# Performance work log

Measured on AMD Instinct MI355X. Metric: run time of the kernel, lower is better.

Reference implementation:

```python
import jax, jax.numpy as jnp
import numpy as np

D = 2048
B, L = 4, 4096

def log_g(x):
    # where(x>=0, log(relu(x)+0.5), -softplus(-x))
    return jnp.where(x >= 0, jnp.log(jax.nn.relu(x) + 0.5), -jax.nn.softplus(-x))

def setup_inputs() -> dict:
    key = jax.random.key(0)
    kx, kz, kn = jax.random.split(key, 3)
    x = jax.random.normal(kx, (B, L, D), dtype=jnp.float32)
    # kaiming_normal for Linear(D, D): std = sqrt(2 / fan_in)
    std = np.sqrt(2.0 / D).astype(np.float32)
    Wz = jax.random.normal(kz, (D, D), dtype=jnp.float32) * std
    Wn = jax.random.normal(kn, (D, D), dtype=jnp.float32) * std
    bz = jnp.zeros((D,), dtype=jnp.float32)
    bn = jnp.zeros((D,), dtype=jnp.float32)
    return {"x": x, "Wz": Wz, "bz": bz, "Wn": Wn, "bn": bn}

def reference(x, Wz, bz, Wn, bn):
    Bq, Lq, Dq = x.shape
    k = jnp.einsum('bld,ed->ble', x, Wz) + bz          # fc_z(x)
    log_z = -jax.nn.softplus(-k)                        # log sigmoid(k)
    log_coeffs = -jax.nn.softplus(k)                    # log(1 - sigmoid(k))
    log_h0 = jnp.full((Bq, 1, Dq), jnp.log(0.5), dtype=x.dtype)  # log_g(0)
    log_h_ = log_g(jnp.einsum('bld,ed->ble', x, Wn) + bn)        # log_g(fc_n(x))
    log_values = jnp.concatenate([log_h0, log_z + log_h_], axis=1)   # (B, L+1, D)
    a_star = jnp.pad(jnp.cumsum(log_coeffs, axis=1), ((0, 0), (1, 0), (0, 0)))  # (B, L+1, D)
    log_h = a_star + jax.lax.cumlogsumexp(log_values - a_star, axis=1)
    return jnp.exp(log_h)[:, 1:]
```

## Files before the change

### kernel.cpp

```cpp
#include <hip/hip_runtime.h>
#include <hip/hip_bf16.h>


#define D_DIM 2048
#define B_DIM 4
#define L_DIM 4096
#define M_DIM (B_DIM * L_DIM)
#define KDIM  D_DIM
#define NCOL  (2 * D_DIM)
#define CHUNK 64
#define NCHUNK (L_DIM / CHUNK)

typedef __bf16 bf16x8 __attribute__((ext_vector_type(8)));
typedef float  f32x4  __attribute__((ext_vector_type(4)));

__device__ __forceinline__ unsigned short f2bf(float f) {
  unsigned int u = __float_as_uint(f);
  u += 0x7FFFu + ((u >> 16) & 1u);
  return (unsigned short)(u >> 16);
}
__device__ __forceinline__ float bf2f(unsigned short s) {
  return __uint_as_float(((unsigned int)s) << 16);
}

__device__ __forceinline__ void load_lds16(const void* g, void* l) {
  __builtin_amdgcn_global_load_lds(
      (const __attribute__((address_space(1))) void*)g,
      (__attribute__((address_space(3))) void*)l, 16, 0, 0);
}

__global__ __launch_bounds__(256) void cast_inputs(
    const float* __restrict__ x, const float* __restrict__ Wz,
    const float* __restrict__ Wn,
    unsigned short* __restrict__ xb, unsigned short* __restrict__ wb) {
  const size_t MK4 = (size_t)M_DIM * KDIM / 4;
  const size_t DD4 = (size_t)D_DIM * D_DIM / 4;
  size_t i = (size_t)blockIdx.x * 256 + threadIdx.x;
  const float4* src; ushort4* dst; size_t off;
  if (i < MK4)            { src = (const float4*)x;  dst = (ushort4*)xb; off = i; }
  else if (i < MK4 + DD4) { src = (const float4*)Wz; dst = (ushort4*)wb; off = i - MK4; }
  else                    { src = (const float4*)Wn;
                            dst = (ushort4*)(wb + (size_t)D_DIM * D_DIM);
                            off = i - MK4 - DD4; }
  float4 v = src[off];
  ushort4 o;
  o.x = f2bf(v.x); o.y = f2bf(v.y); o.z = f2bf(v.z); o.w = f2bf(v.w);
  dst[off] = o;
}

__global__ __launch_bounds__(256) void gemm_fused(
    const unsigned short* __restrict__ xb, const unsigned short* __restrict__ wb,
    const float* __restrict__ bzv, const float* __restrict__ bnv,
    unsigned short* __restrict__ Ab, unsigned short* __restrict__ Gb) {
  __shared__ unsigned short As[128 * 32];
  __shared__ unsigned short Bs[128 * 32];
  const int t = threadIdx.x;
  const int w = t >> 6, lane = t & 63;
  const int ntile = blockIdx.x;
  const int mtile = blockIdx.y;
  const unsigned short* aSrc = xb + (size_t)mtile * 128 * KDIM;
  const unsigned short* bSrc = wb + (size_t)ntile * 128 * KDIM;

  f32x4 acc[4][4] = {};
  const int waveM = (w >> 1) * 64;
  const int waveN = (w & 1) * 64;
  const int r0 = t >> 2, r1 = (t + 256) >> 2, sseg = t & 3;

  for (int k0 = 0; k0 < KDIM; k0 += 32) {
    load_lds16(aSrc + (size_t)r0 * KDIM + k0 + sseg * 8, As + (size_t)t * 8);
    load_lds16(aSrc + (size_t)r1 * KDIM + k0 + sseg * 8, As + (size_t)(t + 256) * 8);
    load_lds16(bSrc + (size_t)r0 * KDIM + k0 + sseg * 8, Bs + (size_t)t * 8);
    load_lds16(bSrc + (size_t)r1 * KDIM + k0 + sseg * 8, Bs + (size_t)(t + 256) * 8);
    __syncthreads();

    bf16x8 aF[4], bF[4];
#pragma unroll
    for (int m = 0; m < 4; ++m)
      aF[m] = *(const bf16x8*)&As[(waveM + m * 16 + (lane & 15)) * 32 + (lane >> 4) * 8];
#pragma unroll
    for (int n = 0; n < 4; ++n)
      bF[n] = *(const bf16x8*)&Bs[(waveN + n * 16 + (lane & 15)) * 32 + (lane >> 4) * 8];
#pragma unroll
    for (int m = 0; m < 4; ++m)
#pragma unroll
      for (int n = 0; n < 4; ++n)
        acc[m][n] = __builtin_amdgcn_mfma_f32_16x16x32_bf16(aF[m], bF[n], acc[m][n], 0, 0, 0);
    __syncthreads();
  }

  const bool isZ = (ntile < 16);
  const int colBase = ntile * 128 + waveN;
  const int rowBase = mtile * 128 + waveM;
#pragma unroll
  for (int n = 0; n < 4; ++n) {
    const int gc = colBase + n * 16 + (lane & 15);
    const int dcol = isZ ? gc : (gc - D_DIM);
    const float bias = isZ ? bzv[dcol] : bnv[dcol];
#pragma unroll
    for (int m = 0; m < 4; ++m) {
      const int gr = rowBase + m * 16 + ((lane >> 4) << 2);
#pragma unroll
      for (int j = 0; j < 4; ++j) {
        const float val = acc[m][n][j] + bias;
        const size_t off = (size_t)(gr + j) * D_DIM + dcol;
        if (isZ) {
          Ab[off] = f2bf(1.0f / (1.0f + __expf(val)));
        } else {
          Gb[off] = f2bf(val >= 0.0f ? val + 0.5f : 1.0f / (1.0f + __expf(-val)));
        }
      }
    }
  }
}

__global__ __launch_bounds__(256) void scan_pass1(
    const unsigned short* __restrict__ Ab, const unsigned short* __restrict__ Gb,
    float* __restrict__ SA, float* __restrict__ SV) {
  const int tid = blockIdx.x * 256 + threadIdx.x;
  const int d = tid & (D_DIM - 1);
  const int c = (tid >> 11) & (NCHUNK - 1);
  const int b = tid >> 17;
  size_t base = ((size_t)b * L_DIM + (size_t)c * CHUNK) * D_DIM + d;
  float Acc = 1.0f, Vcc = 0.0f;
#pragma unroll 8
  for (int i = 0; i < CHUNK; ++i) {
    float a = bf2f(Ab[base + (size_t)i * D_DIM]);
    float g = bf2f(Gb[base + (size_t)i * D_DIM]);
    Vcc = a * Vcc + (1.0f - a) * g;
    Acc *= a;
  }
  SA[tid] = Acc;
  SV[tid] = Vcc;
}

__global__ __launch_bounds__(256) void scan_pass2(
    const float* __restrict__ SA, const float* __restrict__ SV,
    float* __restrict__ H0) {
  const int tid = blockIdx.x * 256 + threadIdx.x;
  const int d = tid & (D_DIM - 1);
  const int b = tid >> 11;
  float h = 0.5f;
  for (int c = 0; c < NCHUNK; ++c) {
    size_t idx = ((size_t)b * NCHUNK + c) * D_DIM + d;
    H0[idx] = h;
    h = SA[idx] * h + SV[idx];
  }
}

__global__ __launch_bounds__(256) void scan_pass3(
    const unsigned short* __restrict__ Ab, const unsigned short* __restrict__ Gb,
    const float* __restrict__ H0, float* __restrict__ out) {
  const int tid = blockIdx.x * 256 + threadIdx.x;
  const int d = tid & (D_DIM - 1);
  const int c = (tid >> 11) & (NCHUNK - 1);
  const int b = tid >> 17;
  size_t base = ((size_t)b * L_DIM + (size_t)c * CHUNK) * D_DIM + d;
  float h = H0[tid];
#pragma unroll 8
  for (int i = 0; i < CHUNK; ++i) {
    float a = bf2f(Ab[base + (size_t)i * D_DIM]);
    float g = bf2f(Gb[base + (size_t)i * D_DIM]);
    h = a * h + (1.0f - a) * g;
    out[base + (size_t)i * D_DIM] = h;
  }
}

extern "C" void kernel_launch(void* const* d_in, const int* in_sizes, int n_in,
                              void* d_out, int out_size, void* d_ws, size_t ws_size,
                              hipStream_t stream) {
  const float* x  = (const float*)d_in[0];
  const float* Wz = (const float*)d_in[1];
  const float* bz = (const float*)d_in[2];
  const float* Wn = (const float*)d_in[3];
  const float* bn = (const float*)d_in[4];
  float* out = (float*)d_out;

  char* ws = (char*)d_ws;
  unsigned short* xb = (unsigned short*)(ws);
  unsigned short* wb = (unsigned short*)(ws + 67108864);
  unsigned short* Ab = (unsigned short*)(ws + 83886080);
  unsigned short* Gb = (unsigned short*)(ws + 150994944);
  float* SA = (float*)(ws + 218103808);
  float* SV = (float*)(ws + 220200960);
  float* H0 = (float*)(ws + 222298112);

  cast_inputs<<<40960, 256, 0, stream>>>(x, Wz, Wn, xb, wb);
  gemm_fused<<<dim3(32, 128), 256, 0, stream>>>(xb, wb, bz, bn, Ab, Gb);
  scan_pass1<<<2048, 256, 0, stream>>>(Ab, Gb, SA, SV);
  scan_pass2<<<32, 256, 0, stream>>>(SA, SV, H0);
  scan_pass3<<<2048, 256, 0, stream>>>(Ab, Gb, H0, out);
}
```

Measured before the change: 659.2 us.

## Rewrite GEMM as 256x256 double-buffered pipelined tile and vectorize scan passes

The GEMM kernel moves from 128x128 tiles with a single LDS buffer and a k-step of 32 to 256x256 tiles with 8 waves, a k-step of 64 and double-buffered LDS. Global-to-LDS loads are staged one and two iterations ahead, LDS layouts are XOR-swizzled, MFMA phases are split into quadrants with barriers and setprio, and block IDs are swizzled. The intent is to overlap memory latency with MFMA work, raise data reuse and avoid LDS bank conflicts. The scan passes now process two adjacent channels per thread using 32-bit loads and float2 stores, which halves the thread count and widens memory accesses.

```diff
diff --git a/kernel.cpp b/kernel.cpp
--- a/kernel.cpp
+++ b/kernel.cpp
@@ -7,7 +7,7 @@
 #define L_DIM 4096
 #define M_DIM (B_DIM * L_DIM)
 #define KDIM  D_DIM
-#define NCOL  (2 * D_DIM)
+#define NT    (KDIM / 64)
 #define CHUNK 64
 #define NCHUNK (L_DIM / CHUNK)
 
@@ -48,89 +48,172 @@
   dst[off] = o;
 }
 
-__global__ __launch_bounds__(256) void gemm_fused(
+__global__ __launch_bounds__(512, 2) void gemm_fused(
     const unsigned short* __restrict__ xb, const unsigned short* __restrict__ wb,
     const float* __restrict__ bzv, const float* __restrict__ bnv,
     unsigned short* __restrict__ Ab, unsigned short* __restrict__ Gb) {
-  __shared__ unsigned short As[128 * 32];
-  __shared__ unsigned short Bs[128 * 32];
+  __shared__ unsigned short lds[2][4][8192];
   const int t = threadIdx.x;
-  const int w = t >> 6, lane = t & 63;
-  const int ntile = blockIdx.x;
-  const int mtile = blockIdx.y;
-  const unsigned short* aSrc = xb + (size_t)mtile * 128 * KDIM;
-  const unsigned short* bSrc = wb + (size_t)ntile * 128 * KDIM;
-
-  f32x4 acc[4][4] = {};
-  const int waveM = (w >> 1) * 64;
-  const int waveN = (w & 1) * 64;
-  const int r0 = t >> 2, r1 = (t + 256) >> 2, sseg = t & 3;
-
-  for (int k0 = 0; k0 < KDIM; k0 += 32) {
-    load_lds16(aSrc + (size_t)r0 * KDIM + k0 + sseg * 8, As + (size_t)t * 8);
-    load_lds16(aSrc + (size_t)r1 * KDIM + k0 + sseg * 8, As + (size_t)(t + 256) * 8);
-    load_lds16(bSrc + (size_t)r0 * KDIM + k0 + sseg * 8, Bs + (size_t)t * 8);
-    load_lds16(bSrc + (size_t)r1 * KDIM + k0 + sseg * 8, Bs + (size_t)(t + 256) * 8);
-    __syncthreads();
-
-    bf16x8 aF[4], bF[4];
-#pragma unroll
-    for (int m = 0; m < 4; ++m)
-      aF[m] = *(const bf16x8*)&As[(waveM + m * 16 + (lane & 15)) * 32 + (lane >> 4) * 8];
-#pragma unroll
-    for (int n = 0; n < 4; ++n)
-      bF[n] = *(const bf16x8*)&Bs[(waveN + n * 16 + (lane & 15)) * 32 + (lane >> 4) * 8];
-#pragma unroll
-    for (int m = 0; m < 4; ++m)
-#pragma unroll
-      for (int n = 0; n < 4; ++n)
-        acc[m][n] = __builtin_amdgcn_mfma_f32_16x16x32_bf16(aF[m], bF[n], acc[m][n], 0, 0, 0);
-    __syncthreads();
-  }
-
-  const bool isZ = (ntile < 16);
-  const int colBase = ntile * 128 + waveN;
-  const int rowBase = mtile * 128 + waveM;
-#pragma unroll
-  for (int n = 0; n < 4; ++n) {
-    const int gc = colBase + n * 16 + (lane & 15);
-    const int dcol = isZ ? gc : (gc - D_DIM);
-    const float bias = isZ ? bzv[dcol] : bnv[dcol];
+  const int lane = t & 63;
+  const int wid = t >> 6;
+  const int wm = wid >> 2, wn = wid & 3;
+  const int laneRow = lane & 15, lg = lane >> 4;
+
+  const int bid = blockIdx.x;
+  const int swz = (bid & 7) * 128 + (bid >> 3);
+  const int mtile = swz >> 4;
+  const int ntile = swz & 15;
+
+  const unsigned short* aBase = xb + (size_t)mtile * 256 * KDIM;
+  const unsigned short* bBase = wb + (size_t)ntile * 256 * KDIM;
+
+  const int r0 = t >> 3;
+  const int sSwz = (t & 7) ^ (r0 & 7);
+
+#define STAGE(buf, reg, srcB, halfRow, kt) do {                                   \
+    const unsigned short* s_ = (srcB) + (size_t)((halfRow) + r0) * KDIM           \
+                               + (kt) * 64 + sSwz * 8;                            \
+    unsigned short* d_ = &lds[buf][reg][t * 8];                                   \
+    load_lds16(s_, d_);                                                           \
+    load_lds16(s_ + 64 * KDIM, d_ + 4096);                                        \
+  } while (0)
+
+  const int sA0 = ((0 + lg) ^ (laneRow & 7)) * 8;
+  const int sA1 = ((4 + lg) ^ (laneRow & 7)) * 8;
+  const int bRow0 = (wn & 1) * 64;
+
+  f32x4 acc[8][4] = {};
+
+  STAGE(0, 2, bBase, 0, 0);  STAGE(0, 3, bBase, 128, 0);
+  STAGE(0, 0, aBase, 0, 0);  STAGE(0, 1, aBase, 128, 0);
+  STAGE(1, 2, bBase, 0, 1);  STAGE(1, 3, bBase, 128, 1);
+  asm volatile("s_waitcnt vmcnt(4)" ::: "memory");
+  __builtin_amdgcn_sched_barrier(0);
+  __builtin_amdgcn_s_barrier();
+
+#define MFMA_QUAD(qm, qn)                                                         \
+  _Pragma("unroll") for (int m = 0; m < 4; ++m)                                   \
+  _Pragma("unroll") for (int n = 0; n < 2; ++n)                                   \
+  _Pragma("unroll") for (int k = 0; k < 2; ++k)                                   \
+    acc[(qm)*4 + m][(qn)*2 + n] = __builtin_amdgcn_mfma_f32_16x16x32_bf16(        \
+        aF[m*2 + k], bF[((qn)*2 + n)*2 + k], acc[(qm)*4 + m][(qn)*2 + n], 0, 0, 0)
+
+  for (int U = 0; U < NT; ++U) {
+    const int cur = U & 1;
+    const unsigned short* ldsA = lds[cur][wm];
+    const unsigned short* ldsB = lds[cur][2 + (wn >> 1)];
+    bf16x8 aF[8], bF[8];
+
 #pragma unroll
     for (int m = 0; m < 4; ++m) {
-      const int gr = rowBase + m * 16 + ((lane >> 4) << 2);
+      aF[m*2+0] = *(const bf16x8*)&ldsA[(m*16 + laneRow) * 64 + sA0];
+      aF[m*2+1] = *(const bf16x8*)&ldsA[(m*16 + laneRow) * 64 + sA1];
+    }
+#pragma unroll
+    for (int n = 0; n < 2; ++n) {
+      bF[n*2+0] = *(const bf16x8*)&ldsB[(bRow0 + n*16 + laneRow) * 64 + sA0];
+      bF[n*2+1] = *(const bf16x8*)&ldsB[(bRow0 + n*16 + laneRow) * 64 + sA1];
+    }
+    if (U + 1 < NT) STAGE(cur ^ 1, 0, aBase, 0, U + 1);
+    __builtin_amdgcn_s_barrier();
+    __builtin_amdgcn_s_setprio(1);
+    MFMA_QUAD(0, 0);
+    __builtin_amdgcn_s_setprio(0);
+    __builtin_amdgcn_s_barrier();
+
+#pragma unroll
+    for (int n = 0; n < 2; ++n) {
+      bF[4 + n*2+0] = *(const bf16x8*)&ldsB[(bRow0 + 32 + n*16 + laneRow) * 64 + sA0];
+      bF[4 + n*2+1] = *(const bf16x8*)&ldsB[(bRow0 + 32 + n*16 + laneRow) * 64 + sA1];
+    }
+    if (U + 1 < NT) STAGE(cur ^ 1, 1, aBase, 128, U + 1);
+    __builtin_amdgcn_s_barrier();
+    __builtin_amdgcn_s_setprio(1);
+    MFMA_QUAD(0, 1);
+    __builtin_amdgcn_s_setprio(0);
+    __builtin_amdgcn_s_barrier();
+
+#pragma unroll
+    for (int m = 0; m < 4; ++m) {
+      aF[m*2+0] = *(const bf16x8*)&ldsA[(64 + m*16 + laneRow) * 64 + sA0];
+      aF[m*2+1] = *(const bf16x8*)&ldsA[(64 + m*16 + laneRow) * 64 + sA1];
+    }
+    if (U + 2 < NT) STAGE(cur, 2, bBase, 0, U + 2);
+    __builtin_amdgcn_s_barrier();
+    __builtin_amdgcn_s_setprio(1);
+    MFMA_QUAD(1, 0);
+    __builtin_amdgcn_s_setprio(0);
+    __builtin_amdgcn_s_barrier();
+
+    if (U + 2 < NT) {
+      STAGE(cur, 3, bBase, 128, U + 2);
+      asm volatile("s_waitcnt vmcnt(4)" ::: "memory");
+      __builtin_amdgcn_sched_barrier(0);
+    } else if (U + 1 < NT) {
+      asm volatile("s_waitcnt vmcnt(0)" ::: "memory");
+      __builtin_amdgcn_sched_barrier(0);
+    }
+    __builtin_amdgcn_s_barrier();
+    __builtin_amdgcn_s_setprio(1);
+    MFMA_QUAD(1, 1);
+    __builtin_amdgcn_s_setprio(0);
+    __builtin_amdgcn_s_barrier();
+  }
+
+  const int gcB = ntile * 256 + wn * 64;
+  const int grB = mtile * 256 + wm * 128;
+  const bool isZ = (ntile < 8);
+  unsigned short* outP = isZ ? Ab : Gb;
+  float bias[4];
+#pragma unroll
+  for (int ni = 0; ni < 4; ++ni) {
+    const int gc = gcB + ni * 16 + laneRow;
+    bias[ni] = isZ ? bzv[gc] : bnv[gc - D_DIM];
+  }
+#pragma unroll
+  for (int mi = 0; mi < 8; ++mi) {
+#pragma unroll
+    for (int ni = 0; ni < 4; ++ni) {
+      const int gc = gcB + ni * 16 + laneRow;
+      const int dcol = isZ ? gc : gc - D_DIM;
 #pragma unroll
       for (int j = 0; j < 4; ++j) {
-        const float val = acc[m][n][j] + bias;
-        const size_t off = (size_t)(gr + j) * D_DIM + dcol;
-        if (isZ) {
-          Ab[off] = f2bf(1.0f / (1.0f + __expf(val)));
-        } else {
-          Gb[off] = f2bf(val >= 0.0f ? val + 0.5f : 1.0f / (1.0f + __expf(-val)));
-        }
+        const float val = acc[mi][ni][j] + bias[ni];
+        const int gr = grB + mi * 16 + (lg << 2) + j;
+        const size_t off = (size_t)gr * D_DIM + dcol;
+        if (isZ) outP[off] = f2bf(1.0f / (1.0f + __expf(val)));
+        else     outP[off] = f2bf(val >= 0.0f ? val + 0.5f
+                                              : 1.0f / (1.0f + __expf(-val)));
       }
     }
   }
+#undef STAGE
+#undef MFMA_QUAD
 }
 
 __global__ __launch_bounds__(256) void scan_pass1(
     const unsigned short* __restrict__ Ab, const unsigned short* __restrict__ Gb,
     float* __restrict__ SA, float* __restrict__ SV) {
   const int tid = blockIdx.x * 256 + threadIdx.x;
-  const int d = tid & (D_DIM - 1);
-  const int c = (tid >> 11) & (NCHUNK - 1);
-  const int b = tid >> 17;
-  size_t base = ((size_t)b * L_DIM + (size_t)c * CHUNK) * D_DIM + d;
-  float Acc = 1.0f, Vcc = 0.0f;
+  const int dp = tid & 1023;
+  const int c = (tid >> 10) & (NCHUNK - 1);
+  const int b = tid >> 16;
+  const unsigned int* A32 = (const unsigned int*)Ab;
+  const unsigned int* G32 = (const unsigned int*)Gb;
+  size_t basePair = ((size_t)b * L_DIM + (size_t)c * CHUNK) * 1024 + dp;
+  float A0 = 1.0f, V0 = 0.0f, A1 = 1.0f, V1 = 0.0f;
 #pragma unroll 8
   for (int i = 0; i < CHUNK; ++i) {
-    float a = bf2f(Ab[base + (size_t)i * D_DIM]);
-    float g = bf2f(Gb[base + (size_t)i * D_DIM]);
-    Vcc = a * Vcc + (1.0f - a) * g;
-    Acc *= a;
-  }
-  SA[tid] = Acc;
-  SV[tid] = Vcc;
+    unsigned int av = A32[basePair + (size_t)i * 1024];
+    unsigned int gv = G32[basePair + (size_t)i * 1024];
+    float a0 = __uint_as_float(av << 16), a1 = __uint_as_float(av & 0xFFFF0000u);
+    float g0 = __uint_as_float(gv << 16), g1 = __uint_as_float(gv & 0xFFFF0000u);
+    V0 = a0 * V0 + (1.0f - a0) * g0;  A0 *= a0;
+    V1 = a1 * V1 + (1.0f - a1) * g1;  A1 *= a1;
+  }
+  const size_t sidx = ((size_t)b * NCHUNK + c) * D_DIM + (size_t)dp * 2;
+  *(float2*)&SA[sidx] = make_float2(A0, A1);
+  *(float2*)&SV[sidx] = make_float2(V0, V1);
 }
 
 __global__ __launch_bounds__(256) void scan_pass2(
@@ -151,17 +234,24 @@
     const unsigned short* __restrict__ Ab, const unsigned short* __restrict__ Gb,
     const float* __restrict__ H0, float* __restrict__ out) {
   const int tid = blockIdx.x * 256 + threadIdx.x;
-  const int d = tid & (D_DIM - 1);
-  const int c = (tid >> 11) & (NCHUNK - 1);
-  const int b = tid >> 17;
-  size_t base = ((size_t)b * L_DIM + (size_t)c * CHUNK) * D_DIM + d;
-  float h = H0[tid];
+  const int dp = tid & 1023;
+  const int c = (tid >> 10) & (NCHUNK - 1);
+  const int b = tid >> 16;
+  const unsigned int* A32 = (const unsigned int*)Ab;
+  const unsigned int* G32 = (const unsigned int*)Gb;
+  size_t basePair = ((size_t)b * L_DIM + (size_t)c * CHUNK) * 1024 + dp;
+  const size_t hidx = ((size_t)b * NCHUNK + c) * D_DIM + (size_t)dp * 2;
+  float2 h2 = *(const float2*)&H0[hidx];
+  float h0 = h2.x, h1 = h2.y;
 #pragma unroll 8
   for (int i = 0; i < CHUNK; ++i) {
-    float a = bf2f(Ab[base + (size_t)i * D_DIM]);
-    float g = bf2f(Gb[base + (size_t)i * D_DIM]);
-    h = a * h + (1.0f - a) * g;
-    out[base + (size_t)i * D_DIM] = h;
+    unsigned int av = A32[basePair + (size_t)i * 1024];
+    unsigned int gv = G32[basePair + (size_t)i * 1024];
+    float a0 = __uint_as_float(av << 16), a1 = __uint_as_float(av & 0xFFFF0000u);
+    float g0 = __uint_as_float(gv << 16), g1 = __uint_as_float(gv & 0xFFFF0000u);
+    h0 = a0 * h0 + (1.0f - a0) * g0;
+    h1 = a1 * h1 + (1.0f - a1) * g1;
+    *(float2*)&out[(basePair + (size_t)i * 1024) * 2] = make_float2(h0, h1);
   }
 }
 
@@ -185,8 +275,8 @@
   float* H0 = (float*)(ws + 222298112);
 
   cast_inputs<<<40960, 256, 0, stream>>>(x, Wz, Wn, xb, wb);
-  gemm_fused<<<dim3(32, 128), 256, 0, stream>>>(xb, wb, bz, bn, Ab, Gb);
-  scan_pass1<<<2048, 256, 0, stream>>>(Ab, Gb, SA, SV);
+  gemm_fused<<<1024, 512, 0, stream>>>(xb, wb, bz, bn, Ab, Gb);
+  scan_pass1<<<1024, 256, 0, stream>>>(Ab, Gb, SA, SV);
   scan_pass2<<<32, 256, 0, stream>>>(SA, SV, H0);
-  scan_pass3<<<2048, 256, 0, stream>>>(Ab, Gb, H0, out);
-}
+  scan_pass3<<<1024, 256, 0, stream>>>(Ab, Gb, H0, out);
+}
```

Result: faster. 576.6 us (-12.5%).
